# Kernel optimization log

Hardware: AMD Instinct MI355X
Metric: run time of the kernel (lower is better)

The kernel has to match this reference:

```python
import jax, jax.numpy as jnp
from jax import lax
import numpy as np

H = 64  # LSTM_HIDDEN


def _lstm_layer(x, Wih, Whh, bih, bhh):
    """PyTorch-convention LSTM layer. x: [B,T,D]; Wih: [4H,D]; Whh: [4H,H]. Gate order i,f,g,o."""
    B = x.shape[0]
    h0 = jnp.zeros((B, H), x.dtype)
    c0 = jnp.zeros((B, H), x.dtype)
    # Precompute input contribution for all timesteps: [T,B,4H]
    xg = jnp.einsum('btd,gd->tbg', x, Wih) + bih + bhh

    def step(carry, xg_t):
        h, c = carry
        gates = xg_t + h @ Whh.T  # [B,4H]
        i, f, g, o = jnp.split(gates, 4, axis=-1)
        i = jax.nn.sigmoid(i)
        f = jax.nn.sigmoid(f)
        g = jnp.tanh(g)
        o = jax.nn.sigmoid(o)
        c = f * c + i * g
        h = o * jnp.tanh(c)
        return (h, c), h

    _, hs = lax.scan(step, (h0, c0), xg)  # hs: [T,B,H]
    return jnp.transpose(hs, (1, 0, 2))  # [B,T,H]


def setup_inputs() -> dict:
    key = jax.random.key(0)
    ks = jax.random.split(key, 12)
    B, T = 1024, 2048
    s = 1.0 / np.sqrt(H)  # PyTorch default uniform init bound
    u = lambda k, shape: jax.random.uniform(k, shape, jnp.float32, -s, s)
    return {
        'x': jax.random.normal(ks[0], (B, T), jnp.float32),
        'Wih0': u(ks[1], (4 * H, 1)),
        'Whh0': u(ks[2], (4 * H, H)),
        'bih0': u(ks[3], (4 * H,)),
        'bhh0': u(ks[4], (4 * H,)),
        'Wih1': u(ks[5], (4 * H, H)),
        'Whh1': u(ks[6], (4 * H, H)),
        'bih1': u(ks[7], (4 * H,)),
        'bhh1': u(ks[8], (4 * H,)),
        'fcW': u(ks[9], (1, H)),
        'fcb': u(ks[10], (1,)),
    }


def reference(x, Wih0, Whh0, bih0, bhh0, Wih1, Whh1, bih1, bhh1, fcW, fcb):
    x = x[..., None]  # unsqueeze(-1) -> [B,T,1]
    h1 = _lstm_layer(x, Wih0, Whh0, bih0, bhh0)   # [B,T,H]
    h2 = _lstm_layer(h1, Wih1, Whh1, bih1, bhh1)  # [B,T,H]
    last = h2[:, -1, :]                            # [B,H]
    logits = last @ fcW.T + fcb                    # [B,1]
    return jnp.squeeze(logits, axis=-1)            # [B]
```

## Files before the change

### kernel.cpp

```cpp
#include <hip/hip_runtime.h>

#define TT 2048
#define HD 64

#define H1_BASE 0
#define H2_BASE 2112
#define FCS_BASE 4160

#define SIC -1.4426950408889634f
#define SGC -2.8853900817779268f

#if __has_builtin(__builtin_amdgcn_exp2f)
#define EXP2F(x) __builtin_amdgcn_exp2f(x)
#else
#define EXP2F(x) __expf(0.69314718055994531f * (x))
#endif
#if __has_builtin(__builtin_amdgcn_rcpf)
#define RCPF(x) __builtin_amdgcn_rcpf(x)
#else
#define RCPF(x) (1.0f / (x))
#endif

__device__ __forceinline__ float rcp1p(float t) { return RCPF(1.0f + EXP2F(t)); }

__device__ __forceinline__ int swz(int b) { return ((b ^ ((b >> 2) & 3)) << 4); }

template<int CTRL>
__device__ __forceinline__ float dpp_get(float v) {
    return __int_as_float(__builtin_amdgcn_update_dpp(0, __float_as_int(v), CTRL, 0xF, 0xF, true));
}

#define BARRIER() asm volatile("s_waitcnt lgkmcnt(0)\n\ts_barrier" ::: "memory")

__device__ __forceinline__ float4 scale4(float4 v, float s) {
    return make_float4(v.x * s, v.y * s, v.z * s, v.w * s);
}

#define DOT16I(acc, W0, W1, W2, W3) \
    acc = W0.x * hv0.x;                acc = __fmaf_rn(W0.y, hv0.y, acc); \
    acc = __fmaf_rn(W0.z, hv0.z, acc); acc = __fmaf_rn(W0.w, hv0.w, acc); \
    acc = __fmaf_rn(W1.x, hv1.x, acc); acc = __fmaf_rn(W1.y, hv1.y, acc); \
    acc = __fmaf_rn(W1.z, hv1.z, acc); acc = __fmaf_rn(W1.w, hv1.w, acc); \
    acc = __fmaf_rn(W2.x, hv2.x, acc); acc = __fmaf_rn(W2.y, hv2.y, acc); \
    acc = __fmaf_rn(W2.z, hv2.z, acc); acc = __fmaf_rn(W2.w, hv2.w, acc); \
    acc = __fmaf_rn(W3.x, hv3.x, acc); acc = __fmaf_rn(W3.y, hv3.y, acc); \
    acc = __fmaf_rn(W3.w, hv3.w, acc); acc = __fmaf_rn(W3.z, hv3.z, acc);

#define ROWDOTI(P, IMM, A0, A1, A2, A3) { \
    const float4 hv0 = *(const float4*)(P##0 + (IMM)); \
    const float4 hv1 = *(const float4*)(P##1 + (IMM)); \
    const float4 hv2 = *(const float4*)(P##2 + (IMM)); \
    const float4 hv3 = *(const float4*)(P##3 + (IMM)); \
    DOT16I(A0, wA0, wA1, wA2, wA3); \
    DOT16I(A1, wB0, wB1, wB2, wB3); \
    DOT16I(A2, wC0, wC1, wC2, wC3); \
    DOT16I(A3, wD0, wD1, wD2, wD3); }

#define QRED(e, r0, r1, r2, r3) \
    float e; { \
        float x_ = q1 ? (r1) : (r0); float y_ = q1 ? (r0) : (r1); \
        x_ += dpp_get<0xB1>(y_); \
        float z_ = q1 ? (r3) : (r2); float w_ = q1 ? (r2) : (r3); \
        z_ += dpp_get<0xB1>(w_); \
        float u_ = q2 ? z_ : x_; float v_ = q2 ? x_ : z_; \
        e = u_ + dpp_get<0x4E>(v_); \
    }

#define STEP(P, X, L0WOFF, L1WOFF, DO_L1, XNI)                                  \
{                                                                               \
    float xv = 0.f;                                                             \
    if (isL0) {                                                                 \
        xv = X;                                                                 \
        const int xi_ = (XNI) < TT ? (XNI) : (TT - 1);                          \
        X = xps[xi_];                                                           \
    }                                                                           \
    float a00, a01, a02, a03, a10, a11, a12, a13;                               \
    float a20, a21, a22, a23, a30, a31, a32, a33;                               \
    ROWDOTI(P, 0 * 256, a00, a01, a02, a03)                                     \
    ROWDOTI(P, 1 * 256, a10, a11, a12, a13)                                     \
    ROWDOTI(P, 2 * 256, a20, a21, a22, a23)                                     \
    ROWDOTI(P, 3 * 256, a30, a31, a32, a33)                                     \
    QRED(e0_, a00, a10, a20, a30)                                               \
    QRED(e1_, a01, a11, a21, a31)                                               \
    QRED(e2_, a02, a12, a22, a32)                                               \
    QRED(e3_, a03, a13, a23, a33)                                               \
    if (isL0) {                                                                 \
        const float iv = rcp1p(__fmaf_rn(xv, wxm0, bgm0) + e0_);                \
        const float fv = rcp1p(__fmaf_rn(xv, wxm1, bgm1) + e1_);                \
        const float gv = __fmaf_rn(2.f, rcp1p(__fmaf_rn(xv, wxm2, bgm2) + e2_), -1.f); \
        const float ov = rcp1p(__fmaf_rn(xv, wxm3, bgm3) + e3_);                \
        cc = __fmaf_rn(fv, cc, iv * gv);                                        \
        const float th = __fmaf_rn(2.f, rcp1p(cc * SGC), -1.f);                 \
        *(float*)(wraddr + (L0WOFF)) = ov * th;                                 \
    } else {                                                                    \
                   \
        e0_ += dpp_get<0x12C>(e0_);                                             \
        e1_ += dpp_get<0x12C>(e1_);                                             \
        e2_ += dpp_get<0x12C>(e2_);                                             \
        e3_ += dpp_get<0x12C>(e3_);                                             \
        if ((DO_L1) && ck < 4) {                                                \
            const float iv = rcp1p(e0_ + bgm0);                                 \
            const float fv = rcp1p(e1_ + bgm1);                                 \
            const float gv = __fmaf_rn(2.f, rcp1p(e2_ + bgm2), -1.f);           \
            const float ov = rcp1p(e3_ + bgm3);                                 \
            cc = __fmaf_rn(fv, cc, iv * gv);                                    \
            hlast = ov * __fmaf_rn(2.f, rcp1p(cc * SGC), -1.f);                 \
            *(float*)(wraddr + (L1WOFF)) = hlast;                               \
        }                                                                       \
    }                                                                           \
    BARRIER();                                                                  \
}

__global__ __launch_bounds__(768, 3)
void lstm2_kernel(const float* __restrict__ x,
                  const float* __restrict__ Wih0,
                  const float* __restrict__ Whh0,
                  const float* __restrict__ bih0,
                  const float* __restrict__ bhh0,
                  const float* __restrict__ Wih1,
                  const float* __restrict__ Whh1,
                  const float* __restrict__ bih1,
                  const float* __restrict__ bhh1,
                  const float* __restrict__ fcW,
                  const float* __restrict__ fcb,
                  float* __restrict__ out)
{
    __shared__ __align__(16) float arena_f[1296];
    char* const arena = (char*)arena_f;

    const int tid  = threadIdx.x;
    const int row0 = blockIdx.x * 4;

    const bool isL0 = (tid < 256);
    const int  p    = isL0 ? tid : (tid - 256);
    const int  j    = isL0 ? (p >> 2) : (p >> 3);
    const int  ck   = isL0 ? (p & 3)  : (p & 7);
    const int  ckk  = (ck < 4) ? ck : (ck - 4);
    const int  rk   = ck & 3;
    const bool q1   = (rk & 1) != 0;
    const bool q2   = (rk & 2) != 0;

    const float* Wsrc;
    if (isL0)        Wsrc = Whh0;
    else if (ck < 4) Wsrc = Wih1;
    else             Wsrc = Whh1;
    const int kbase = 16 * ckk;
    const float4* W0p = (const float4*)(Wsrc + (0 * HD + j) * HD + kbase);
    const float4* W1p = (const float4*)(Wsrc + (1 * HD + j) * HD + kbase);
    const float4* W2p = (const float4*)(Wsrc + (2 * HD + j) * HD + kbase);
    const float4* W3p = (const float4*)(Wsrc + (3 * HD + j) * HD + kbase);
    const float4 wA0 = scale4(W0p[0], SIC), wA1 = scale4(W0p[1], SIC),
                 wA2 = scale4(W0p[2], SIC), wA3 = scale4(W0p[3], SIC);
    const float4 wB0 = scale4(W1p[0], SIC), wB1 = scale4(W1p[1], SIC),
                 wB2 = scale4(W1p[2], SIC), wB3 = scale4(W1p[3], SIC);
    const float4 wC0 = scale4(W2p[0], SGC), wC1 = scale4(W2p[1], SGC),
                 wC2 = scale4(W2p[2], SGC), wC3 = scale4(W2p[3], SGC);
    const float4 wD0 = scale4(W3p[0], SIC), wD1 = scale4(W3p[1], SIC),
                 wD2 = scale4(W3p[2], SIC), wD3 = scale4(W3p[3], SIC);

    float bgm0, bgm1, bgm2, bgm3, wxm0 = 0.f, wxm1 = 0.f, wxm2 = 0.f, wxm3 = 0.f;
    if (isL0) {
        bgm0 = (bih0[0*HD+j] + bhh0[0*HD+j]) * SIC;
        bgm1 = (bih0[1*HD+j] + bhh0[1*HD+j]) * SIC;
        bgm2 = (bih0[2*HD+j] + bhh0[2*HD+j]) * SGC;
        bgm3 = (bih0[3*HD+j] + bhh0[3*HD+j]) * SIC;
        wxm0 = Wih0[0*HD+j] * SIC;
        wxm1 = Wih0[1*HD+j] * SIC;
        wxm2 = Wih0[2*HD+j] * SGC;
        wxm3 = Wih0[3*HD+j] * SIC;
    } else {
        bgm0 = (bih1[0*HD+j] + bhh1[0*HD+j]) * SIC;
        bgm1 = (bih1[1*HD+j] + bhh1[1*HD+j]) * SIC;
        bgm2 = (bih1[2*HD+j] + bhh1[2*HD+j]) * SGC;
        bgm3 = (bih1[3*HD+j] + bhh1[3*HD+j]) * SIC;
    }

    const int o0 = swz(4 * ckk + 0);
    const int o1 = swz(4 * ckk + 1);
    const int o2 = swz(4 * ckk + 2);
    const int o3 = swz(4 * ckk + 3);
    const int rdBase = (ck < 4) ? H1_BASE : H2_BASE;
    const int rdPh   = (ck < 4) ? 1 : 0;

    const char* pe0 = arena + rdBase + (rdPh << 10) + o0;
    const char* pe1 = arena + rdBase + (rdPh << 10) + o1;
    const char* pe2 = arena + rdBase + (rdPh << 10) + o2;
    const char* pe3 = arena + rdBase + (rdPh << 10) + o3;
    const char* po0 = arena + rdBase + ((rdPh ^ 1) << 10) + o0;
    const char* po1 = arena + rdBase + ((rdPh ^ 1) << 10) + o1;
    const char* po2 = arena + rdBase + ((rdPh ^ 1) << 10) + o2;
    const char* po3 = arena + rdBase + ((rdPh ^ 1) << 10) + o3;

    char* const wraddr = arena + (isL0 ? H1_BASE : H2_BASE)
                       + ((ck & 3) << 8) + swz(j >> 2) + ((j & 3) << 2);

    for (int z = tid; z < 512; z += 768) {
        *(float*)(arena + H1_BASE + 4 * z) = 0.f;
        *(float*)(arena + H2_BASE + 4 * z) = 0.f;
    }

    const float* xps = x + (row0 + rk) * TT;
    float xa = 0.f, xb = 0.f;
    if (isL0) { xa = xps[0]; xb = xps[1]; }

    const float fcwj = fcW[j];
    float cc = 0.f, hlast = 0.f;

    __syncthreads();

    STEP(pe, xa, 0, 1024, false, 2)
    STEP(po, xb, 1024, 0, true, 3)
#pragma unroll 1
    for (int i = 2; i < TT; i += 2) {
        STEP(pe, xa, 0, 1024, true, i + 2)
        STEP(po, xb, 1024, 0, true, i + 3)
    }
    if (!isL0) {
        float a00, a01, a02, a03, a10, a11, a12, a13;
        float a20, a21, a22, a23, a30, a31, a32, a33;
        ROWDOTI(pe, 0 * 256, a00, a01, a02, a03)
        ROWDOTI(pe, 1 * 256, a10, a11, a12, a13)
        ROWDOTI(pe, 2 * 256, a20, a21, a22, a23)
        ROWDOTI(pe, 3 * 256, a30, a31, a32, a33)
        QRED(e0_, a00, a10, a20, a30)
        QRED(e1_, a01, a11, a21, a31)
        QRED(e2_, a02, a12, a22, a32)
        QRED(e3_, a03, a13, a23, a33)
        e0_ += dpp_get<0x12C>(e0_);
        e1_ += dpp_get<0x12C>(e1_);
        e2_ += dpp_get<0x12C>(e2_);
        e3_ += dpp_get<0x12C>(e3_);
        if (ck < 4) {
            const float iv = rcp1p(e0_ + bgm0);
            const float fv = rcp1p(e1_ + bgm1);
            const float gv = __fmaf_rn(2.f, rcp1p(e2_ + bgm2), -1.f);
            const float ov = rcp1p(e3_ + bgm3);
            cc = __fmaf_rn(fv, cc, iv * gv);
            hlast = ov * __fmaf_rn(2.f, rcp1p(cc * SGC), -1.f);
        }
    }
    __syncthreads();

    if (!isL0 && ck < 4)
        *(float*)(arena + FCS_BASE + ((ck * HD + j) << 2)) = hlast * fcwj;
    __syncthreads();

    if (tid < 64) {
        const int r = tid >> 4, seg = tid & 15;
        const float4 v = ((const float4*)(arena + FCS_BASE))[r * 16 + seg];
        float s = (v.x + v.y) + (v.z + v.w);
        s += __shfl_xor(s, 1, 64);
        s += __shfl_xor(s, 2, 64);
        s += __shfl_xor(s, 4, 64);
        s += __shfl_xor(s, 8, 64);
        if (seg == 0) out[row0 + r] = s + fcb[0];
    }
}

extern "C" void kernel_launch(void* const* d_in, const int* in_sizes, int n_in,
                              void* d_out, int out_size, void* d_ws, size_t ws_size,
                              hipStream_t stream) {
    const float* x    = (const float*)d_in[0];
    const float* Wih0 = (const float*)d_in[1];
    const float* Whh0 = (const float*)d_in[2];
    const float* bih0 = (const float*)d_in[3];
    const float* bhh0 = (const float*)d_in[4];
    const float* Wih1 = (const float*)d_in[5];
    const float* Whh1 = (const float*)d_in[6];
    const float* bih1 = (const float*)d_in[7];
    const float* bhh1 = (const float*)d_in[8];
    const float* fcW  = (const float*)d_in[9];
    const float* fcb  = (const float*)d_in[10];
    float* out = (float*)d_out;

    lstm2_kernel<<<256, 768, 0, stream>>>(x, Wih0, Whh0, bih0, bhh0,
                                          Wih1, Whh1, bih1, bhh1,
                                          fcW, fcb, out);
}
```

Measured before the change: 2.913 ms.

## Store hidden state and weights in fp16 and use packed fdot2 dot products

Converts the recurrent weights to packed half-precision pairs held in registers and stores hidden states in shared memory as fp16. The per-gate dot products now use v_dot2 instructions, which halves the FMA count, and each lane reads half as many LDS bytes per step. The LDS layout is rebuilt with padded row strides in place of the XOR swizzle, and the arena shrinks. The cost is reduced numerical precision across 2048 recurrent steps, plus possible bank conflicts from the new layout.

```diff
diff --git a/kernel.cpp b/kernel.cpp
--- a/kernel.cpp
+++ b/kernel.cpp
@@ -4,8 +4,10 @@
 #define HD 64
 
 #define H1_BASE 0
-#define H2_BASE 2112
-#define FCS_BASE 4160
+#define H2_BASE 1344
+#define FCS_BASE 2624
+#define PSTR 640
+#define RSTR 160
 
 #define SIC -1.4426950408889634f
 #define SGC -2.8853900817779268f
@@ -23,7 +25,18 @@
 
 __device__ __forceinline__ float rcp1p(float t) { return RCPF(1.0f + EXP2F(t)); }
 
-__device__ __forceinline__ int swz(int b) { return ((b ^ ((b >> 2) & 3)) << 4); }
+typedef _Float16 v2h __attribute__((ext_vector_type(2)));
+
+#if __has_builtin(__builtin_amdgcn_fdot2)
+#define FDOT2(a, b, c) __builtin_amdgcn_fdot2((a), (b), (c), false)
+#else
+#define FDOT2(a, b, c) __fmaf_rn((float)(a)[1], (float)(b)[1], __fmaf_rn((float)(a)[0], (float)(b)[0], (c)))
+#endif
+
+static __device__ __forceinline__ v2h bch(float f) { return __builtin_bit_cast(v2h, f); }
+static __device__ __forceinline__ v2h packw(float a, float b, float s) {
+    v2h r; r[0] = (_Float16)(a * s); r[1] = (_Float16)(b * s); return r;
+}
 
 template<int CTRL>
 __device__ __forceinline__ float dpp_get(float v) {
@@ -32,29 +45,25 @@
 
 #define BARRIER() asm volatile("s_waitcnt lgkmcnt(0)\n\ts_barrier" ::: "memory")
 
-__device__ __forceinline__ float4 scale4(float4 v, float s) {
-    return make_float4(v.x * s, v.y * s, v.z * s, v.w * s);
-}
-
-#define DOT16I(acc, W0, W1, W2, W3) \
-    acc = W0.x * hv0.x;                acc = __fmaf_rn(W0.y, hv0.y, acc); \
-    acc = __fmaf_rn(W0.z, hv0.z, acc); acc = __fmaf_rn(W0.w, hv0.w, acc); \
-    acc = __fmaf_rn(W1.x, hv1.x, acc); acc = __fmaf_rn(W1.y, hv1.y, acc); \
-    acc = __fmaf_rn(W1.z, hv1.z, acc); acc = __fmaf_rn(W1.w, hv1.w, acc); \
-    acc = __fmaf_rn(W2.x, hv2.x, acc); acc = __fmaf_rn(W2.y, hv2.y, acc); \
-    acc = __fmaf_rn(W2.z, hv2.z, acc); acc = __fmaf_rn(W2.w, hv2.w, acc); \
-    acc = __fmaf_rn(W3.x, hv3.x, acc); acc = __fmaf_rn(W3.y, hv3.y, acc); \
-    acc = __fmaf_rn(W3.w, hv3.w, acc); acc = __fmaf_rn(W3.z, hv3.z, acc);
-
-#define ROWDOTI(P, IMM, A0, A1, A2, A3) { \
-    const float4 hv0 = *(const float4*)(P##0 + (IMM)); \
-    const float4 hv1 = *(const float4*)(P##1 + (IMM)); \
-    const float4 hv2 = *(const float4*)(P##2 + (IMM)); \
-    const float4 hv3 = *(const float4*)(P##3 + (IMM)); \
-    DOT16I(A0, wA0, wA1, wA2, wA3); \
-    DOT16I(A1, wB0, wB1, wB2, wB3); \
-    DOT16I(A2, wC0, wC1, wC2, wC3); \
-    DOT16I(A3, wD0, wD1, wD2, wD3); }
+#define GDOT8I(acc, W) \
+    acc = FDOT2(W##0, h0_, 0.0f); \
+    acc = FDOT2(W##1, h1_, acc);  \
+    acc = FDOT2(W##2, h2_, acc);  \
+    acc = FDOT2(W##3, h3_, acc);  \
+    acc = FDOT2(W##4, h4_, acc);  \
+    acc = FDOT2(W##5, h5_, acc);  \
+    acc = FDOT2(W##6, h6_, acc);  \
+    acc = FDOT2(W##7, h7_, acc);
+
+#define ROWDOTH(P, ROFF, A0, A1, A2, A3) { \
+    const float4 f0_ = *(const float4*)(P##0 + (ROFF)); \
+    const float4 f1_ = *(const float4*)(P##1 + (ROFF)); \
+    const v2h h0_ = bch(f0_.x), h1_ = bch(f0_.y), h2_ = bch(f0_.z), h3_ = bch(f0_.w); \
+    const v2h h4_ = bch(f1_.x), h5_ = bch(f1_.y), h6_ = bch(f1_.z), h7_ = bch(f1_.w); \
+    GDOT8I(A0, wA) \
+    GDOT8I(A1, wB) \
+    GDOT8I(A2, wC) \
+    GDOT8I(A3, wD) }
 
 #define QRED(e, r0, r1, r2, r3) \
     float e; { \
@@ -76,10 +85,10 @@
     }                                                                           \
     float a00, a01, a02, a03, a10, a11, a12, a13;                               \
     float a20, a21, a22, a23, a30, a31, a32, a33;                               \
-    ROWDOTI(P, 0 * 256, a00, a01, a02, a03)                                     \
-    ROWDOTI(P, 1 * 256, a10, a11, a12, a13)                                     \
-    ROWDOTI(P, 2 * 256, a20, a21, a22, a23)                                     \
-    ROWDOTI(P, 3 * 256, a30, a31, a32, a33)                                     \
+    ROWDOTH(P, 0 * RSTR, a00, a01, a02, a03)                                    \
+    ROWDOTH(P, 1 * RSTR, a10, a11, a12, a13)                                    \
+    ROWDOTH(P, 2 * RSTR, a20, a21, a22, a23)                                    \
+    ROWDOTH(P, 3 * RSTR, a30, a31, a32, a33)                                    \
     QRED(e0_, a00, a10, a20, a30)                                               \
     QRED(e1_, a01, a11, a21, a31)                                               \
     QRED(e2_, a02, a12, a22, a32)                                               \
@@ -91,7 +100,7 @@
         const float ov = rcp1p(__fmaf_rn(xv, wxm3, bgm3) + e3_);                \
         cc = __fmaf_rn(fv, cc, iv * gv);                                        \
         const float th = __fmaf_rn(2.f, rcp1p(cc * SGC), -1.f);                 \
-        *(float*)(wraddr + (L0WOFF)) = ov * th;                                 \
+        *(_Float16*)(wraddr + (L0WOFF)) = (_Float16)(ov * th);                  \
     } else {                                                                    \
                    \
         e0_ += dpp_get<0x12C>(e0_);                                             \
@@ -105,7 +114,7 @@
             const float ov = rcp1p(e3_ + bgm3);                                 \
             cc = __fmaf_rn(fv, cc, iv * gv);                                    \
             hlast = ov * __fmaf_rn(2.f, rcp1p(cc * SGC), -1.f);                 \
-            *(float*)(wraddr + (L1WOFF)) = hlast;                               \
+            *(_Float16*)(wraddr + (L1WOFF)) = (_Float16)hlast;                  \
         }                                                                       \
     }                                                                           \
     BARRIER();                                                                  \
@@ -125,7 +134,7 @@
                   const float* __restrict__ fcb,
                   float* __restrict__ out)
 {
-    __shared__ __align__(16) float arena_f[1296];
+    __shared__ __align__(16) float arena_f[912];
     char* const arena = (char*)arena_f;
 
     const int tid  = threadIdx.x;
@@ -145,18 +154,26 @@
     else if (ck < 4) Wsrc = Wih1;
     else             Wsrc = Whh1;
     const int kbase = 16 * ckk;
-    const float4* W0p = (const float4*)(Wsrc + (0 * HD + j) * HD + kbase);
-    const float4* W1p = (const float4*)(Wsrc + (1 * HD + j) * HD + kbase);
-    const float4* W2p = (const float4*)(Wsrc + (2 * HD + j) * HD + kbase);
-    const float4* W3p = (const float4*)(Wsrc + (3 * HD + j) * HD + kbase);
-    const float4 wA0 = scale4(W0p[0], SIC), wA1 = scale4(W0p[1], SIC),
-                 wA2 = scale4(W0p[2], SIC), wA3 = scale4(W0p[3], SIC);
-    const float4 wB0 = scale4(W1p[0], SIC), wB1 = scale4(W1p[1], SIC),
-                 wB2 = scale4(W1p[2], SIC), wB3 = scale4(W1p[3], SIC);
-    const float4 wC0 = scale4(W2p[0], SGC), wC1 = scale4(W2p[1], SGC),
-                 wC2 = scale4(W2p[2], SGC), wC3 = scale4(W2p[3], SGC);
-    const float4 wD0 = scale4(W3p[0], SIC), wD1 = scale4(W3p[1], SIC),
-                 wD2 = scale4(W3p[2], SIC), wD3 = scale4(W3p[3], SIC);
+    const float* Wg0 = Wsrc + (0 * HD + j) * HD + kbase;
+    const float* Wg1 = Wsrc + (1 * HD + j) * HD + kbase;
+    const float* Wg2 = Wsrc + (2 * HD + j) * HD + kbase;
+    const float* Wg3 = Wsrc + (3 * HD + j) * HD + kbase;
+    const v2h wA0 = packw(Wg0[0],  Wg0[1],  SIC), wA1 = packw(Wg0[2],  Wg0[3],  SIC),
+              wA2 = packw(Wg0[4],  Wg0[5],  SIC), wA3 = packw(Wg0[6],  Wg0[7],  SIC),
+              wA4 = packw(Wg0[8],  Wg0[9],  SIC), wA5 = packw(Wg0[10], Wg0[11], SIC),
+              wA6 = packw(Wg0[12], Wg0[13], SIC), wA7 = packw(Wg0[14], Wg0[15], SIC);
+    const v2h wB0 = packw(Wg1[0],  Wg1[1],  SIC), wB1 = packw(Wg1[2],  Wg1[3],  SIC),
+              wB2 = packw(Wg1[4],  Wg1[5],  SIC), wB3 = packw(Wg1[6],  Wg1[7],  SIC),
+              wB4 = packw(Wg1[8],  Wg1[9],  SIC), wB5 = packw(Wg1[10], Wg1[11], SIC),
+              wB6 = packw(Wg1[12], Wg1[13], SIC), wB7 = packw(Wg1[14], Wg1[15], SIC);
+    const v2h wC0 = packw(Wg2[0],  Wg2[1],  SGC), wC1 = packw(Wg2[2],  Wg2[3],  SGC),
+              wC2 = packw(Wg2[4],  Wg2[5],  SGC), wC3 = packw(Wg2[6],  Wg2[7],  SGC),
+              wC4 = packw(Wg2[8],  Wg2[9],  SGC), wC5 = packw(Wg2[10], Wg2[11], SGC),
+              wC6 = packw(Wg2[12], Wg2[13], SGC), wC7 = packw(Wg2[14], Wg2[15], SGC);
+    const v2h wD0 = packw(Wg3[0],  Wg3[1],  SIC), wD1 = packw(Wg3[2],  Wg3[3],  SIC),
+              wD2 = packw(Wg3[4],  Wg3[5],  SIC), wD3 = packw(Wg3[6],  Wg3[7],  SIC),
+              wD4 = packw(Wg3[8],  Wg3[9],  SIC), wD5 = packw(Wg3[10], Wg3[11], SIC),
+              wD6 = packw(Wg3[12], Wg3[13], SIC), wD7 = packw(Wg3[14], Wg3[15], SIC);
 
     float bgm0, bgm1, bgm2, bgm3, wxm0 = 0.f, wxm1 = 0.f, wxm2 = 0.f, wxm3 = 0.f;
     if (isL0) {
@@ -175,29 +192,19 @@
         bgm3 = (bih1[3*HD+j] + bhh1[3*HD+j]) * SIC;
     }
 
-    const int o0 = swz(4 * ckk + 0);
-    const int o1 = swz(4 * ckk + 1);
-    const int o2 = swz(4 * ckk + 2);
-    const int o3 = swz(4 * ckk + 3);
     const int rdBase = (ck < 4) ? H1_BASE : H2_BASE;
     const int rdPh   = (ck < 4) ? 1 : 0;
-
-    const char* pe0 = arena + rdBase + (rdPh << 10) + o0;
-    const char* pe1 = arena + rdBase + (rdPh << 10) + o1;
-    const char* pe2 = arena + rdBase + (rdPh << 10) + o2;
-    const char* pe3 = arena + rdBase + (rdPh << 10) + o3;
-    const char* po0 = arena + rdBase + ((rdPh ^ 1) << 10) + o0;
-    const char* po1 = arena + rdBase + ((rdPh ^ 1) << 10) + o1;
-    const char* po2 = arena + rdBase + ((rdPh ^ 1) << 10) + o2;
-    const char* po3 = arena + rdBase + ((rdPh ^ 1) << 10) + o3;
-
-    char* const wraddr = arena + (isL0 ? H1_BASE : H2_BASE)
-                       + ((ck & 3) << 8) + swz(j >> 2) + ((j & 3) << 2);
-
-    for (int z = tid; z < 512; z += 768) {
-        *(float*)(arena + H1_BASE + 4 * z) = 0.f;
-        *(float*)(arena + H2_BASE + 4 * z) = 0.f;
-    }
+    const int coff   = ckk * 32;
+
+    const char* pe0 = arena + rdBase + rdPh * PSTR + coff;
+    const char* pe1 = pe0 + 16;
+    const char* po0 = arena + rdBase + (rdPh ^ 1) * PSTR + coff;
+    const char* po1 = po0 + 16;
+
+    char* const wraddr = arena + (isL0 ? H1_BASE : H2_BASE) + rk * RSTR + (j << 1);
+
+    for (int z = tid; z < 656; z += 768)
+        *(float*)(arena + 4 * z) = 0.f;
 
     const float* xps = x + (row0 + rk) * TT;
     float xa = 0.f, xb = 0.f;
@@ -208,20 +215,20 @@
 
     __syncthreads();
 
-    STEP(pe, xa, 0, 1024, false, 2)
-    STEP(po, xb, 1024, 0, true, 3)
+    STEP(pe, xa, 0, PSTR, false, 2)
+    STEP(po, xb, PSTR, 0, true, 3)
 #pragma unroll 1
     for (int i = 2; i < TT; i += 2) {
-        STEP(pe, xa, 0, 1024, true, i + 2)
-        STEP(po, xb, 1024, 0, true, i + 3)
+        STEP(pe, xa, 0, PSTR, true, i + 2)
+        STEP(po, xb, PSTR, 0, true, i + 3)
     }
     if (!isL0) {
         float a00, a01, a02, a03, a10, a11, a12, a13;
         float a20, a21, a22, a23, a30, a31, a32, a33;
-        ROWDOTI(pe, 0 * 256, a00, a01, a02, a03)
-        ROWDOTI(pe, 1 * 256, a10, a11, a12, a13)
-        ROWDOTI(pe, 2 * 256, a20, a21, a22, a23)
-        ROWDOTI(pe, 3 * 256, a30, a31, a32, a33)
+        ROWDOTH(pe, 0 * RSTR, a00, a01, a02, a03)
+        ROWDOTH(pe, 1 * RSTR, a10, a11, a12, a13)
+        ROWDOTH(pe, 2 * RSTR, a20, a21, a22, a23)
+        ROWDOTH(pe, 3 * RSTR, a30, a31, a32, a33)
         QRED(e0_, a00, a10, a20, a30)
         QRED(e1_, a01, a11, a21, a31)
         QRED(e2_, a02, a12, a22, a32)
@@ -242,7 +249,7 @@
     __syncthreads();
 
     if (!isL0 && ck < 4)
-        *(float*)(arena + FCS_BASE + ((ck * HD + j) << 2)) = hlast * fcwj;
+        *(float*)(arena + FCS_BASE + ((rk * HD + j) << 2)) = hlast * fcwj;
     __syncthreads();
 
     if (tid < 64) {
```

After: 2.796 ms. 4.0% less time.
